# Optimization experiments

Hardware: AMD Instinct MI355X
Metric: run time of the kernel (lower is better)

The kernel has to match this reference:

```python
import jax, jax.numpy as jnp
import numpy as np

LAMBDA_DRO = 0.1
EPSILON = 0.5
EPS = 1e-8

N, M, D, K = 2048, 4096, 512, 1000


def _cosine_matrix(a, b):
    # a: [N, d], b: [M, d] -> [N, M] cosine similarity via normalize + GEMM
    an = a / jnp.maximum(jnp.linalg.norm(a, axis=1, keepdims=True), EPS)
    bn = b / jnp.maximum(jnp.linalg.norm(b, axis=1, keepdims=True), EPS)
    return an @ bn.T


def setup_inputs() -> dict:
    key = jax.random.key(0)
    k = jax.random.split(key, 7)
    return {
        "ptr_features": jax.random.normal(k[0], (N, D), dtype=jnp.float32),
        "ptr_logits": jax.random.normal(k[1], (N, K), dtype=jnp.float32),
        "ptr_labels": jax.random.randint(k[2], (N,), 0, K),
        "nu_features": jax.random.normal(k[3], (M, D), dtype=jnp.float32),
        "nu_logits": jax.random.normal(k[4], (M, K), dtype=jnp.float32),
        "nu_labels": jax.random.randint(k[5], (M,), 0, K),
        "classifier_weights": jax.random.normal(k[6], (K, D), dtype=jnp.float32),
    }


def reference(ptr_features, ptr_logits, ptr_labels, nu_features, nu_logits,
              nu_labels, classifier_weights):
    # per-sample CE loss on nu (hard labels)
    log_probs = jax.nn.log_softmax(nu_logits, axis=1)          # [M, K]
    nu_losses = -jnp.take_along_axis(log_probs, nu_labels[:, None], axis=1)[:, 0]  # [M]

    # transport costs
    C_X = 1.0 - _cosine_matrix(ptr_features, nu_features)       # [N, M]
    ptr_emb = classifier_weights[ptr_labels]                    # [N, d]
    nu_emb = classifier_weights[nu_labels]                      # [M, d]
    C_Y = 1.0 - _cosine_matrix(ptr_emb, nu_emb)                 # [N, M]
    C_total = C_X + C_Y

    # worst-case distribution Q^lambda
    exponent = (nu_losses[None, :] - LAMBDA_DRO * C_total) / (LAMBDA_DRO * EPSILON + EPS)
    exponent = exponent - jnp.max(exponent, axis=1, keepdims=True)
    exp_terms = jnp.exp(exponent)                               # [N, M]
    weights = exp_terms / (jnp.sum(exp_terms, axis=1, keepdims=True) + EPS)
    probs = jnp.mean(weights, axis=0)                           # [M]
    probs = probs / (jnp.sum(probs) + EPS)

    dro_loss = jnp.sum(probs * nu_losses)
    total_loss = dro_loss  # semantic_loss = 0 (no moco inputs)
    return (total_loss, dro_loss, probs, jnp.mean(C_total), jnp.mean(C_X), jnp.mean(C_Y))
```

## Files before the change

### kernel.cpp

```cpp
#include <hip/hip_runtime.h>
#include <math.h>

#define N_PTR 2048
#define M_NU  4096
#define DIM   512
#define KCLS  1000
#define KPAD  1024

static constexpr float LAMBDA_ = 0.1f;
static constexpr float EPS_ = 1e-8f;
static constexpr float INV_DENOM = 1.0f / (0.1f * 0.5f + 1e-8f);

typedef short short8 __attribute__((ext_vector_type(8)));
typedef unsigned short u16x8 __attribute__((ext_vector_type(8)));
typedef float f32x4 __attribute__((ext_vector_type(4)));

__device__ __forceinline__ unsigned short f2bf(float x) {
  unsigned u = __float_as_uint(x);
  u += 0x7fff + ((u >> 16) & 1);
  return (unsigned short)(u >> 16);
}
__device__ __forceinline__ float bf2f(unsigned short h) {
  return __uint_as_float(((unsigned)h) << 16);
}

__device__ __forceinline__ void gload16(const void* g, void* l) {
  __builtin_amdgcn_global_load_lds(
      (const __attribute__((address_space(1))) unsigned int*)g,
      (__attribute__((address_space(3))) unsigned int*)l, 16, 0, 0);
}

__device__ __forceinline__ float blk_reduce_sum(float v, float* red) {
  #pragma unroll
  for (int off = 32; off > 0; off >>= 1) v += __shfl_down(v, off);
  __syncthreads();
  if ((threadIdx.x & 63) == 0) red[threadIdx.x >> 6] = v;
  __syncthreads();
  return red[0] + red[1] + red[2] + red[3];
}

__device__ __forceinline__ float blk_reduce_max(float v, float* red) {
  #pragma unroll
  for (int off = 32; off > 0; off >>= 1) v = fmaxf(v, __shfl_down(v, off));
  __syncthreads();
  if ((threadIdx.x & 63) == 0) red[threadIdx.x >> 6] = v;
  __syncthreads();
  return fmaxf(fmaxf(red[0], red[1]), fmaxf(red[2], red[3]));
}

__global__ __launch_bounds__(256) void prep_kernel(
    const float* __restrict__ ptr_f, const float* __restrict__ nu_f,
    const float* __restrict__ cls_f, const float* __restrict__ logits,
    const int* __restrict__ labels, unsigned short* __restrict__ An,
    unsigned short* __restrict__ Bn, unsigned short* __restrict__ Cn,
    float* __restrict__ losses) {
  __shared__ float red[4];
  int b = blockIdx.x;
  if (b < 1792) {
    int gid = b * 256 + threadIdx.x;
    int row = gid >> 6, lane = gid & 63;
    const float* src; unsigned short* dst; int lrow; int in_rows;
    if (row < N_PTR)             { src = ptr_f; dst = An; lrow = row;                in_rows = N_PTR; }
    else if (row < N_PTR + M_NU) { src = nu_f;  dst = Bn; lrow = row - N_PTR;        in_rows = M_NU; }
    else                         { src = cls_f; dst = Cn; lrow = row - N_PTR - M_NU; in_rows = KCLS; }
    u16x8 ov;
    if (lrow < in_rows) {
      const float4* rp = (const float4*)(src + (size_t)lrow * DIM);
      float4 a = rp[lane * 2], bq = rp[lane * 2 + 1];
      float v[8] = {a.x, a.y, a.z, a.w, bq.x, bq.y, bq.z, bq.w};
      float s = 0.f;
      #pragma unroll
      for (int j = 0; j < 8; ++j) s = fmaf(v[j], v[j], s);
      #pragma unroll
      for (int off = 32; off > 0; off >>= 1) s += __shfl_xor(s, off);
      float inv = 1.0f / fmaxf(sqrtf(s), EPS_);
      #pragma unroll
      for (int j = 0; j < 8; ++j) ov[j] = f2bf(v[j] * inv);
    } else {
      #pragma unroll
      for (int j = 0; j < 8; ++j) ov[j] = 0;
    }
    *(u16x8*)(dst + (size_t)lrow * DIM + lane * 8) = ov;
  } else {
    int row = b - 1792;
    int tid = threadIdx.x;
    const float* x = logits + (size_t)row * KCLS;
    const float4* x4 = (const float4*)x;
    float4 v = make_float4(0.f, 0.f, 0.f, 0.f);
    float mx_loc = -INFINITY;
    if (tid < 250) {
      v = x4[tid];
      mx_loc = fmaxf(fmaxf(v.x, v.y), fmaxf(v.z, v.w));
    }
    float mx = blk_reduce_max(mx_loc, red);
    float se_loc = 0.f;
    if (tid < 250)
      se_loc = __expf(v.x - mx) + __expf(v.y - mx) + __expf(v.z - mx) + __expf(v.w - mx);
    float se = blk_reduce_sum(se_loc, red);
    if (tid == 0) losses[row] = mx + logf(se) - x[labels[row]];
  }
}

template <int BM, int MODE>
__global__ __launch_bounds__(256) void mfma_gemm(
    const unsigned short* __restrict__ A, const unsigned short* __restrict__ B,
    unsigned short* __restrict__ Gfb, unsigned short* __restrict__ Tb,
    const int* __restrict__ pl, const int* __restrict__ nl,
    const float* __restrict__ nu_loss, unsigned* __restrict__ gbits,
    float* __restrict__ pr, float* __restrict__ pr2,
    float* __restrict__ s_part, float* __restrict__ gy_part, int ldc) {
  constexpr int FR = BM / 32;
  constexpr int WSPAN = BM / 2;
  __shared__ unsigned short Alds[BM * 64];
  __shared__ unsigned short Blds[BM * 64];
  __shared__ float red[4];
  const int tid = threadIdx.x;
  const int w = tid >> 6, lane = tid & 63;
  const int brow = blockIdx.y * BM, bcol = blockIdx.x * BM;
  const int wr = w >> 1, wc = w & 1;

  if (MODE == 0 && blockIdx.x == 0 && blockIdx.y == 0) {
    float mloc = 0.f;
    for (int i = tid; i < M_NU; i += 256) mloc = fmaxf(mloc, nu_loss[i]);
    float mx = blk_reduce_max(mloc, red);
    if (tid == 0) *gbits = __float_as_uint(mx);
    __syncthreads();
  }

  const int sr = lane >> 3;
  const int sc = lane & 7;
  const int schunk = (sc ^ sr) * 8;

  f32x4 acc[FR][FR] = {};

  for (int k0 = 0; k0 < DIM; k0 += 64) {
    #pragma unroll
    for (int i = 0; i < FR; ++i) {
      int j = w * FR + i;
      int r = j * 8 + sr;
      gload16(A + (size_t)(brow + r) * DIM + k0 + schunk, (char*)Alds + j * 1024);
      gload16(B + (size_t)(bcol + r) * DIM + k0 + schunk, (char*)Blds + j * 1024);
    }
    __syncthreads();
    #pragma unroll
    for (int kk = 0; kk < 2; ++kk) {
      const int koff = kk * 64 + (lane >> 4) * 16;
      short8 af[FR], bfr[FR];
      #pragma unroll
      for (int mi = 0; mi < FR; ++mi) {
        int r = wr * WSPAN + mi * 16 + (lane & 15);
        af[mi] = *(const short8*)((const char*)Alds + r * 128 + (koff ^ ((r & 7) << 4)));
      }
      #pragma unroll
      for (int ni = 0; ni < FR; ++ni) {
        int r = wc * WSPAN + ni * 16 + (lane & 15);
        bfr[ni] = *(const short8*)((const char*)Blds + r * 128 + (koff ^ ((r & 7) << 4)));
      }
      #pragma unroll
      for (int mi = 0; mi < FR; ++mi)
        #pragma unroll
        for (int ni = 0; ni < FR; ++ni)
          acc[mi][ni] = __builtin_amdgcn_mfma_f32_16x16x32_bf16(af[mi], bfr[ni], acc[mi][ni], 0, 0, 0);
    }
    __syncthreads();
  }

  if (MODE == 0) {
    #pragma unroll
    for (int mi = 0; mi < FR; ++mi)
      #pragma unroll
      for (int ni = 0; ni < FR; ++ni)
        #pragma unroll
        for (int j = 0; j < 4; ++j) {
          int row = brow + wr * WSPAN + mi * 16 + (lane >> 4) * 4 + j;
          int col = bcol + wc * WSPAN + ni * 16 + (lane & 15);
          Gfb[(size_t)row * ldc + col] = f2bf(acc[mi][ni][j]);
        }
  } else {
    const float gmax = __uint_as_float(*gbits);
    const float fac = LAMBDA_ * INV_DENOM;
    int cols[FR]; float a_r[FR]; float loss_r[FR]; int nl_r[FR];
    #pragma unroll
    for (int ni = 0; ni < FR; ++ni) {
      cols[ni]  = bcol + wc * WSPAN + ni * 16 + (lane & 15);
      loss_r[ni] = nu_loss[cols[ni]];
      a_r[ni]   = (loss_r[ni] - gmax - 2.f * LAMBDA_) * INV_DENOM;
      nl_r[ni]  = nl[cols[ni]];
    }
    float s_acc = 0.f, gy_acc = 0.f;
    #pragma unroll
    for (int mi = 0; mi < FR; ++mi) {
      #pragma unroll
      for (int j = 0; j < 4; ++j) {
        int row = brow + wr * WSPAN + mi * 16 + (lane >> 4) * 4 + j;
        const unsigned short* Grow = Gfb + (size_t)pl[row] * KPAD;
        float rowacc = 0.f, rowacc2 = 0.f;
        #pragma unroll
        for (int ni = 0; ni < FR; ++ni) {
          float s  = acc[mi][ni][j];
          float gy = bf2f(Grow[nl_r[ni]]);
          float e  = fmaf(fac, s + gy, a_r[ni]);
          float t  = __expf(e);
          unsigned short tb = f2bf(t);
          Tb[(size_t)row * ldc + cols[ni]] = tb;
          float tt = bf2f(tb);
          rowacc  += tt;
          rowacc2 += tt * loss_r[ni];
          s_acc += s; gy_acc += gy;
        }
        #pragma unroll
        for (int off = 1; off < 16; off <<= 1) {
          rowacc  += __shfl_xor(rowacc, off);
          rowacc2 += __shfl_xor(rowacc2, off);
        }
        if ((lane & 15) == 0) {
          pr [(size_t)(blockIdx.x * 2 + wc) * N_PTR + row] = rowacc;
          pr2[(size_t)(blockIdx.x * 2 + wc) * N_PTR + row] = rowacc2;
        }
      }
    }
    float stot = blk_reduce_sum(s_acc, red);
    float gtot = blk_reduce_sum(gy_acc, red);
    if (tid == 0) {
      int bid = blockIdx.y * gridDim.x + blockIdx.x;
      s_part[bid] = stot; gy_part[bid] = gtot;
    }
  }
}

__global__ __launch_bounds__(256) void colpass_td_kernel(
    const unsigned short* __restrict__ Tb, const float* __restrict__ pr,
    const float* __restrict__ pr2, float* __restrict__ partial,
    float* __restrict__ T_part, float* __restrict__ D_part) {
  __shared__ float sh[64];
  int b = blockIdx.x, tid = threadIdx.x;
  if (b < 256) {
    int bx = b & 7, by = b >> 3;
    int m0 = bx * 512 + tid * 2;
    int n0 = by * 64;
    if (tid < 64) {
      float rs = 0.f;
      #pragma unroll 4
      for (int cb = 0; cb < 64; ++cb) rs += pr[(size_t)cb * N_PTR + n0 + tid];
      sh[tid] = 1.0f / (rs + EPS_);
    }
    __syncthreads();
    float a0 = 0.f, a1 = 0.f;
    #pragma unroll 4
    for (int i = 0; i < 64; ++i) {
      unsigned tv = *(const unsigned*)(Tb + (size_t)(n0 + i) * M_NU + m0);
      float wv = sh[i];
      a0 = fmaf(bf2f((unsigned short)(tv & 0xffffu)), wv, a0);
      a1 = fmaf(bf2f((unsigned short)(tv >> 16)), wv, a1);
    }
    *(float2*)(partial + (size_t)by * M_NU + m0) = make_float2(a0, a1);
  } else {
    int n = (b - 256) * 128 + (tid & 127);
    float tl = 0.f, dl = 0.f;
    if (tid < 128) {
      float rs = 0.f, wl = 0.f;
      #pragma unroll 4
      for (int cb = 0; cb < 64; ++cb) {
        rs += pr [(size_t)cb * N_PTR + n];
        wl += pr2[(size_t)cb * N_PTR + n];
      }
      float wi = 1.0f / (rs + EPS_);
      tl = rs * wi; dl = wl * wi;
    }
    __syncthreads();
    #pragma unroll
    for (int off = 32; off > 0; off >>= 1) { tl += __shfl_down(tl, off); dl += __shfl_down(dl, off); }
    if ((tid & 63) == 0) { sh[tid >> 6] = tl; sh[4 + (tid >> 6)] = dl; }
    __syncthreads();
    if (tid == 0) {
      T_part[b - 256] = sh[0] + sh[1] + sh[2] + sh[3];
      D_part[b - 256] = sh[4] + sh[5] + sh[6] + sh[7];
    }
  }
}

__global__ __launch_bounds__(256) void final_kernel(const float* __restrict__ partial,
    const float* __restrict__ T_part, const float* __restrict__ D_part,
    const float* __restrict__ s_part, const float* __restrict__ gy_part,
    float* __restrict__ out) {
  __shared__ float red[4];
  int b = blockIdx.x, tid = threadIdx.x;
  float T = 0.f;
  #pragma unroll
  for (int i = 0; i < 16; ++i) T += T_part[i];
  float scale = (1.0f / (float)N_PTR) / (T / (float)N_PTR + EPS_);
  if (b < 16) {
    int m = b * 256 + tid;
    float raw = 0.f;
    #pragma unroll
    for (int c = 0; c < 32; ++c) raw += partial[(size_t)c * M_NU + m];
    out[2 + m] = raw * scale;
  } else {
    float D = 0.f;
    #pragma unroll
    for (int i = 0; i < 16; ++i) D += D_part[i];
    float ls = 0.f, lg = 0.f;
    for (int i = tid; i < 512; i += 256) { ls += s_part[i]; lg += gy_part[i]; }
    float S  = blk_reduce_sum(ls, red);
    float Gy = blk_reduce_sum(lg, red);
    if (tid == 0) {
      float dro = D * scale;
      const float invNM = 1.0f / ((float)N_PTR * (float)M_NU);
      float mcx = 1.f - S * invNM;
      float mcy = 1.f - Gy * invNM;
      out[0] = dro;
      out[1] = dro;
      out[2 + M_NU] = mcx + mcy;
      out[3 + M_NU] = mcx;
      out[4 + M_NU] = mcy;
    }
  }
}

extern "C" void kernel_launch(void* const* d_in, const int* in_sizes, int n_in,
                              void* d_out, int out_size, void* d_ws, size_t ws_size,
                              hipStream_t stream) {
  const float* ptr_feat = (const float*)d_in[0];
  const int*   ptr_lab  = (const int*)d_in[2];
  const float* nu_feat  = (const float*)d_in[3];
  const float* nu_log   = (const float*)d_in[4];
  const int*   nu_lab   = (const int*)d_in[5];
  const float* cls_w    = (const float*)d_in[6];
  float* out = (float*)d_out;

  char* base = (char*)d_ws;
  unsigned short* Tb  = (unsigned short*)base;
  unsigned short* Gfb = (unsigned short*)(base + 16u * 1024 * 1024);
  unsigned short* An  = (unsigned short*)(base + 18u * 1024 * 1024);
  unsigned short* Bn  = (unsigned short*)(base + 20u * 1024 * 1024);
  unsigned short* Cn  = (unsigned short*)(base + 24u * 1024 * 1024);
  float* fb           = (float*)(base + 25u * 1024 * 1024);
  float* nloss   = fb;
  unsigned* gbits= (unsigned*)(nloss + 4096);
  float* pr      = nloss + 4096 + 64;
  float* pr2     = pr  + 64 * N_PTR;
  float* partial = pr2 + 64 * N_PTR;
  float* s_part  = partial + 32 * M_NU;
  float* gy_part = s_part + 512;
  float* T_part  = gy_part + 512;
  float* D_part  = T_part + 16;

  prep_kernel<<<dim3(1792 + M_NU), 256, 0, stream>>>(
      ptr_feat, nu_feat, cls_w, nu_log, nu_lab, An, Bn, Cn, nloss);
  mfma_gemm<64, 0><<<dim3(KPAD / 64, KPAD / 64), 256, 0, stream>>>(
      Cn, Cn, Gfb, nullptr, nullptr, nullptr, nloss, gbits,
      nullptr, nullptr, nullptr, nullptr, KPAD);
  mfma_gemm<128, 1><<<dim3(M_NU / 128, N_PTR / 128), 256, 0, stream>>>(
      An, Bn, Gfb, Tb, ptr_lab, nu_lab, nloss, gbits,
      pr, pr2, s_part, gy_part, M_NU);
  colpass_td_kernel<<<dim3(272), 256, 0, stream>>>(Tb, pr, pr2, partial, T_part, D_part);
  final_kernel<<<dim3(17), 256, 0, stream>>>(partial, T_part, D_part, s_part, gy_part, out);
}
```

Baseline: 62.79 us.

## Fold class-embedding cosine into main GEMM via concatenated K; compute means from column sums

Replaces the separate class-class Gram GEMM and per-element gathers of Gy with a gather of normalized class embeddings per sample (Ae, Be). The main GEMM then accumulates over both feature and embedding halves, giving S+Gy directly. The means of C_X and C_Y are computed from the dot product of column sums (sum_i a_i · sum_j b_j) in a small colsum kernel instead of in the GEMM epilogue. This removes the gathered bf16 lookups and the per-tile reductions from the epilogue, but doubles the GEMM K dimension and adds prep work for the 6144 gathered rows.

```diff
diff --git a/kernel.cpp b/kernel.cpp
--- a/kernel.cpp
+++ b/kernel.cpp
@@ -5,7 +5,6 @@
 #define M_NU  4096
 #define DIM   512
 #define KCLS  1000
-#define KPAD  1024
 
 static constexpr float LAMBDA_ = 0.1f;
 static constexpr float EPS_ = 1e-8f;
@@ -51,39 +50,45 @@
 __global__ __launch_bounds__(256) void prep_kernel(
     const float* __restrict__ ptr_f, const float* __restrict__ nu_f,
     const float* __restrict__ cls_f, const float* __restrict__ logits,
-    const int* __restrict__ labels, unsigned short* __restrict__ An,
-    unsigned short* __restrict__ Bn, unsigned short* __restrict__ Cn,
+    const int* __restrict__ pl, const int* __restrict__ nl,
+    const int* __restrict__ labels,
+    unsigned short* __restrict__ An, unsigned short* __restrict__ Bn,
+    unsigned short* __restrict__ Ae, unsigned short* __restrict__ Be,
     float* __restrict__ losses) {
   __shared__ float red[4];
   int b = blockIdx.x;
-  if (b < 1792) {
-    int gid = b * 256 + threadIdx.x;
+  int tid = threadIdx.x;
+  if (b < 3072) {
+    int gid = b * 256 + tid;
     int row = gid >> 6, lane = gid & 63;
-    const float* src; unsigned short* dst; int lrow; int in_rows;
-    if (row < N_PTR)             { src = ptr_f; dst = An; lrow = row;                in_rows = N_PTR; }
-    else if (row < N_PTR + M_NU) { src = nu_f;  dst = Bn; lrow = row - N_PTR;        in_rows = M_NU; }
-    else                         { src = cls_f; dst = Cn; lrow = row - N_PTR - M_NU; in_rows = KCLS; }
+    const float* src; unsigned short* dst;
+    if (row < N_PTR) {
+      src = ptr_f + (size_t)row * DIM;           dst = An + (size_t)row * DIM;
+    } else if (row < N_PTR + M_NU) {
+      int r = row - N_PTR;
+      src = nu_f + (size_t)r * DIM;              dst = Bn + (size_t)r * DIM;
+    } else if (row < N_PTR + M_NU + N_PTR) {
+      int r = row - N_PTR - M_NU;
+      src = cls_f + (size_t)pl[r] * DIM;         dst = Ae + (size_t)r * DIM;
+    } else {
+      int r = row - N_PTR - M_NU - N_PTR;
+      src = cls_f + (size_t)nl[r] * DIM;         dst = Be + (size_t)r * DIM;
+    }
+    const float4* rp = (const float4*)src;
+    float4 a = rp[lane * 2], bq = rp[lane * 2 + 1];
+    float v[8] = {a.x, a.y, a.z, a.w, bq.x, bq.y, bq.z, bq.w};
+    float s = 0.f;
+    #pragma unroll
+    for (int j = 0; j < 8; ++j) s = fmaf(v[j], v[j], s);
+    #pragma unroll
+    for (int off = 32; off > 0; off >>= 1) s += __shfl_xor(s, off);
+    float inv = 1.0f / fmaxf(sqrtf(s), EPS_);
     u16x8 ov;
-    if (lrow < in_rows) {
-      const float4* rp = (const float4*)(src + (size_t)lrow * DIM);
-      float4 a = rp[lane * 2], bq = rp[lane * 2 + 1];
-      float v[8] = {a.x, a.y, a.z, a.w, bq.x, bq.y, bq.z, bq.w};
-      float s = 0.f;
-      #pragma unroll
-      for (int j = 0; j < 8; ++j) s = fmaf(v[j], v[j], s);
-      #pragma unroll
-      for (int off = 32; off > 0; off >>= 1) s += __shfl_xor(s, off);
-      float inv = 1.0f / fmaxf(sqrtf(s), EPS_);
-      #pragma unroll
-      for (int j = 0; j < 8; ++j) ov[j] = f2bf(v[j] * inv);
-    } else {
-      #pragma unroll
-      for (int j = 0; j < 8; ++j) ov[j] = 0;
-    }
-    *(u16x8*)(dst + (size_t)lrow * DIM + lane * 8) = ov;
+    #pragma unroll
+    for (int j = 0; j < 8; ++j) ov[j] = f2bf(v[j] * inv);
+    *(u16x8*)(dst + lane * 8) = ov;
   } else {
-    int row = b - 1792;
-    int tid = threadIdx.x;
+    int row = b - 3072;
     const float* x = logits + (size_t)row * KCLS;
     const float4* x4 = (const float4*)x;
     float4 v = make_float4(0.f, 0.f, 0.f, 0.f);
@@ -101,129 +106,124 @@
   }
 }
 
-template <int BM, int MODE>
-__global__ __launch_bounds__(256) void mfma_gemm(
-    const unsigned short* __restrict__ A, const unsigned short* __restrict__ B,
-    unsigned short* __restrict__ Gfb, unsigned short* __restrict__ Tb,
-    const int* __restrict__ pl, const int* __restrict__ nl,
-    const float* __restrict__ nu_loss, unsigned* __restrict__ gbits,
-    float* __restrict__ pr, float* __restrict__ pr2,
-    float* __restrict__ s_part, float* __restrict__ gy_part, int ldc) {
-  constexpr int FR = BM / 32;
-  constexpr int WSPAN = BM / 2;
-  __shared__ unsigned short Alds[BM * 64];
-  __shared__ unsigned short Blds[BM * 64];
+__global__ __launch_bounds__(256) void colsum_kernel(
+    const unsigned short* __restrict__ An, const unsigned short* __restrict__ Bn,
+    const unsigned short* __restrict__ Ae, const unsigned short* __restrict__ Be,
+    const float* __restrict__ nloss, float* __restrict__ csum_part,
+    unsigned* __restrict__ gbits) {
   __shared__ float red[4];
+  int b = blockIdx.x, tid = threadIdx.x;
+  if (b == 96) {
+    float mloc = 0.f;
+    for (int i = tid; i < M_NU; i += 256) mloc = fmaxf(mloc, nloss[i]);
+    float mx = blk_reduce_max(mloc, red);
+    if (tid == 0) *gbits = __float_as_uint(mx);
+    return;
+  }
+  const unsigned short* basep; int n0;
+  if (b < 16)      { basep = An; n0 = b * 128; }
+  else if (b < 48) { basep = Bn; n0 = (b - 16) * 128; }
+  else if (b < 64) { basep = Ae; n0 = (b - 48) * 128; }
+  else             { basep = Be; n0 = (b - 64) * 128; }
+  float a0 = 0.f, a1 = 0.f;
+  for (int i = 0; i < 128; ++i) {
+    unsigned v = *(const unsigned*)(basep + (size_t)(n0 + i) * DIM + tid * 2);
+    a0 += bf2f((unsigned short)(v & 0xffffu));
+    a1 += bf2f((unsigned short)(v >> 16));
+  }
+  csum_part[(size_t)b * DIM + tid * 2]     = a0;
+  csum_part[(size_t)b * DIM + tid * 2 + 1] = a1;
+}
+
+__global__ __launch_bounds__(256) void sgemm_kernel(
+    const unsigned short* __restrict__ An, const unsigned short* __restrict__ Bn,
+    const unsigned short* __restrict__ Ae, const unsigned short* __restrict__ Be,
+    unsigned short* __restrict__ Tb, const int* __restrict__ nl,
+    const float* __restrict__ nu_loss, const unsigned* __restrict__ gbits,
+    float* __restrict__ pr, float* __restrict__ pr2) {
+  __shared__ unsigned short Alds[128 * 64];
+  __shared__ unsigned short Blds[128 * 64];
   const int tid = threadIdx.x;
   const int w = tid >> 6, lane = tid & 63;
-  const int brow = blockIdx.y * BM, bcol = blockIdx.x * BM;
+  const int brow = blockIdx.y * 128, bcol = blockIdx.x * 128;
   const int wr = w >> 1, wc = w & 1;
-
-  if (MODE == 0 && blockIdx.x == 0 && blockIdx.y == 0) {
-    float mloc = 0.f;
-    for (int i = tid; i < M_NU; i += 256) mloc = fmaxf(mloc, nu_loss[i]);
-    float mx = blk_reduce_max(mloc, red);
-    if (tid == 0) *gbits = __float_as_uint(mx);
-    __syncthreads();
-  }
 
   const int sr = lane >> 3;
   const int sc = lane & 7;
   const int schunk = (sc ^ sr) * 8;
 
-  f32x4 acc[FR][FR] = {};
-
-  for (int k0 = 0; k0 < DIM; k0 += 64) {
-    #pragma unroll
-    for (int i = 0; i < FR; ++i) {
-      int j = w * FR + i;
-      int r = j * 8 + sr;
-      gload16(A + (size_t)(brow + r) * DIM + k0 + schunk, (char*)Alds + j * 1024);
-      gload16(B + (size_t)(bcol + r) * DIM + k0 + schunk, (char*)Blds + j * 1024);
-    }
-    __syncthreads();
-    #pragma unroll
-    for (int kk = 0; kk < 2; ++kk) {
-      const int koff = kk * 64 + (lane >> 4) * 16;
-      short8 af[FR], bfr[FR];
+  f32x4 acc[4][4] = {};
+
+  #pragma unroll
+  for (int half = 0; half < 2; ++half) {
+    const unsigned short* Ab = half ? Ae : An;
+    const unsigned short* Bb = half ? Be : Bn;
+    for (int k0 = 0; k0 < DIM; k0 += 64) {
       #pragma unroll
-      for (int mi = 0; mi < FR; ++mi) {
-        int r = wr * WSPAN + mi * 16 + (lane & 15);
-        af[mi] = *(const short8*)((const char*)Alds + r * 128 + (koff ^ ((r & 7) << 4)));
-      }
+      for (int i = 0; i < 4; ++i) {
+        int j = w * 4 + i;
+        int r = j * 8 + sr;
+        gload16(Ab + (size_t)(brow + r) * DIM + k0 + schunk, (char*)Alds + j * 1024);
+        gload16(Bb + (size_t)(bcol + r) * DIM + k0 + schunk, (char*)Blds + j * 1024);
+      }
+      __syncthreads();
       #pragma unroll
-      for (int ni = 0; ni < FR; ++ni) {
-        int r = wc * WSPAN + ni * 16 + (lane & 15);
-        bfr[ni] = *(const short8*)((const char*)Blds + r * 128 + (koff ^ ((r & 7) << 4)));
-      }
-      #pragma unroll
-      for (int mi = 0; mi < FR; ++mi)
+      for (int kk = 0; kk < 2; ++kk) {
+        const int koff = kk * 64 + (lane >> 4) * 16;
+        short8 af[4], bfr[4];
         #pragma unroll
-        for (int ni = 0; ni < FR; ++ni)
-          acc[mi][ni] = __builtin_amdgcn_mfma_f32_16x16x32_bf16(af[mi], bfr[ni], acc[mi][ni], 0, 0, 0);
-    }
-    __syncthreads();
-  }
-
-  if (MODE == 0) {
-    #pragma unroll
-    for (int mi = 0; mi < FR; ++mi)
-      #pragma unroll
-      for (int ni = 0; ni < FR; ++ni)
-        #pragma unroll
-        for (int j = 0; j < 4; ++j) {
-          int row = brow + wr * WSPAN + mi * 16 + (lane >> 4) * 4 + j;
-          int col = bcol + wc * WSPAN + ni * 16 + (lane & 15);
-          Gfb[(size_t)row * ldc + col] = f2bf(acc[mi][ni][j]);
-        }
-  } else {
-    const float gmax = __uint_as_float(*gbits);
-    const float fac = LAMBDA_ * INV_DENOM;
-    int cols[FR]; float a_r[FR]; float loss_r[FR]; int nl_r[FR];
-    #pragma unroll
-    for (int ni = 0; ni < FR; ++ni) {
-      cols[ni]  = bcol + wc * WSPAN + ni * 16 + (lane & 15);
-      loss_r[ni] = nu_loss[cols[ni]];
-      a_r[ni]   = (loss_r[ni] - gmax - 2.f * LAMBDA_) * INV_DENOM;
-      nl_r[ni]  = nl[cols[ni]];
-    }
-    float s_acc = 0.f, gy_acc = 0.f;
-    #pragma unroll
-    for (int mi = 0; mi < FR; ++mi) {
-      #pragma unroll
-      for (int j = 0; j < 4; ++j) {
-        int row = brow + wr * WSPAN + mi * 16 + (lane >> 4) * 4 + j;
-        const unsigned short* Grow = Gfb + (size_t)pl[row] * KPAD;
-        float rowacc = 0.f, rowacc2 = 0.f;
-        #pragma unroll
-        for (int ni = 0; ni < FR; ++ni) {
-          float s  = acc[mi][ni][j];
-          float gy = bf2f(Grow[nl_r[ni]]);
-          float e  = fmaf(fac, s + gy, a_r[ni]);
-          float t  = __expf(e);
-          unsigned short tb = f2bf(t);
-          Tb[(size_t)row * ldc + cols[ni]] = tb;
-          float tt = bf2f(tb);
-          rowacc  += tt;
-          rowacc2 += tt * loss_r[ni];
-          s_acc += s; gy_acc += gy;
+        for (int mi = 0; mi < 4; ++mi) {
+          int r = wr * 64 + mi * 16 + (lane & 15);
+          af[mi] = *(const short8*)((const char*)Alds + r * 128 + (koff ^ ((r & 7) << 4)));
         }
         #pragma unroll
-        for (int off = 1; off < 16; off <<= 1) {
-          rowacc  += __shfl_xor(rowacc, off);
-          rowacc2 += __shfl_xor(rowacc2, off);
+        for (int ni = 0; ni < 4; ++ni) {
+          int r = wc * 64 + ni * 16 + (lane & 15);
+          bfr[ni] = *(const short8*)((const char*)Blds + r * 128 + (koff ^ ((r & 7) << 4)));
         }
-        if ((lane & 15) == 0) {
-          pr [(size_t)(blockIdx.x * 2 + wc) * N_PTR + row] = rowacc;
-          pr2[(size_t)(blockIdx.x * 2 + wc) * N_PTR + row] = rowacc2;
-        }
-      }
-    }
-    float stot = blk_reduce_sum(s_acc, red);
-    float gtot = blk_reduce_sum(gy_acc, red);
-    if (tid == 0) {
-      int bid = blockIdx.y * gridDim.x + blockIdx.x;
-      s_part[bid] = stot; gy_part[bid] = gtot;
+        #pragma unroll
+        for (int mi = 0; mi < 4; ++mi)
+          #pragma unroll
+          for (int ni = 0; ni < 4; ++ni)
+            acc[mi][ni] = __builtin_amdgcn_mfma_f32_16x16x32_bf16(af[mi], bfr[ni], acc[mi][ni], 0, 0, 0);
+      }
+      __syncthreads();
+    }
+  }
+
+  const float gmax = __uint_as_float(*gbits);
+  const float fac = LAMBDA_ * INV_DENOM;
+  int cols[4]; float a_r[4]; float loss_r[4];
+  #pragma unroll
+  for (int ni = 0; ni < 4; ++ni) {
+    cols[ni]   = bcol + wc * 64 + ni * 16 + (lane & 15);
+    loss_r[ni] = nu_loss[cols[ni]];
+    a_r[ni]    = (loss_r[ni] - gmax - 2.f * LAMBDA_) * INV_DENOM;
+  }
+  #pragma unroll
+  for (int mi = 0; mi < 4; ++mi) {
+    #pragma unroll
+    for (int j = 0; j < 4; ++j) {
+      int row = brow + wr * 64 + mi * 16 + (lane >> 4) * 4 + j;
+      float rowacc = 0.f, rowacc2 = 0.f;
+      #pragma unroll
+      for (int ni = 0; ni < 4; ++ni) {
+        float t = __expf(fmaf(fac, acc[mi][ni][j], a_r[ni]));
+        unsigned short tb = f2bf(t);
+        Tb[(size_t)row * M_NU + cols[ni]] = tb;
+        float tt = bf2f(tb);
+        rowacc  += tt;
+        rowacc2 += tt * loss_r[ni];
+      }
+      #pragma unroll
+      for (int off = 1; off < 16; off <<= 1) {
+        rowacc  += __shfl_xor(rowacc, off);
+        rowacc2 += __shfl_xor(rowacc2, off);
+      }
+      if ((lane & 15) == 0) {
+        pr [(size_t)(blockIdx.x * 2 + wc) * N_PTR + row] = rowacc;
+        pr2[(size_t)(blockIdx.x * 2 + wc) * N_PTR + row] = rowacc2;
+      }
     }
   }
 }
@@ -281,8 +281,7 @@
 
 __global__ __launch_bounds__(256) void final_kernel(const float* __restrict__ partial,
     const float* __restrict__ T_part, const float* __restrict__ D_part,
-    const float* __restrict__ s_part, const float* __restrict__ gy_part,
-    float* __restrict__ out) {
+    const float* __restrict__ csum_part, float* __restrict__ out) {
   __shared__ float red[4];
   int b = blockIdx.x, tid = threadIdx.x;
   float T = 0.f;
@@ -299,15 +298,27 @@
     float D = 0.f;
     #pragma unroll
     for (int i = 0; i < 16; ++i) D += D_part[i];
-    float ls = 0.f, lg = 0.f;
-    for (int i = tid; i < 512; i += 256) { ls += s_part[i]; lg += gy_part[i]; }
-    float S  = blk_reduce_sum(ls, red);
-    float Gy = blk_reduce_sum(lg, red);
+    float lx = 0.f, ly = 0.f;
+    for (int c = tid; c < DIM; c += 256) {
+      float sA = 0.f, sB = 0.f, sPe = 0.f, sQe = 0.f;
+      #pragma unroll 4
+      for (int p = 0; p < 16; ++p)  sA  += csum_part[(size_t)p * DIM + c];
+      #pragma unroll 4
+      for (int p = 16; p < 48; ++p) sB  += csum_part[(size_t)p * DIM + c];
+      #pragma unroll 4
+      for (int p = 48; p < 64; ++p) sPe += csum_part[(size_t)p * DIM + c];
+      #pragma unroll 4
+      for (int p = 64; p < 96; ++p) sQe += csum_part[(size_t)p * DIM + c];
+      lx = fmaf(sA, sB, lx);
+      ly = fmaf(sPe, sQe, ly);
+    }
+    float dX = blk_reduce_sum(lx, red);
+    float dY = blk_reduce_sum(ly, red);
     if (tid == 0) {
       float dro = D * scale;
       const float invNM = 1.0f / ((float)N_PTR * (float)M_NU);
-      float mcx = 1.f - S * invNM;
-      float mcy = 1.f - Gy * invNM;
+      float mcx = 1.f - dX * invNM;
+      float mcy = 1.f - dY * invNM;
       out[0] = dro;
       out[1] = dro;
       out[2 + M_NU] = mcx + mcy;
@@ -329,30 +340,27 @@
   float* out = (float*)d_out;
 
   char* base = (char*)d_ws;
-  unsigned short* Tb  = (unsigned short*)base;
-  unsigned short* Gfb = (unsigned short*)(base + 16u * 1024 * 1024);
-  unsigned short* An  = (unsigned short*)(base + 18u * 1024 * 1024);
-  unsigned short* Bn  = (unsigned short*)(base + 20u * 1024 * 1024);
-  unsigned short* Cn  = (unsigned short*)(base + 24u * 1024 * 1024);
-  float* fb           = (float*)(base + 25u * 1024 * 1024);
-  float* nloss   = fb;
-  unsigned* gbits= (unsigned*)(nloss + 4096);
-  float* pr      = nloss + 4096 + 64;
-  float* pr2     = pr  + 64 * N_PTR;
-  float* partial = pr2 + 64 * N_PTR;
-  float* s_part  = partial + 32 * M_NU;
-  float* gy_part = s_part + 512;
-  float* T_part  = gy_part + 512;
-  float* D_part  = T_part + 16;
-
-  prep_kernel<<<dim3(1792 + M_NU), 256, 0, stream>>>(
-      ptr_feat, nu_feat, cls_w, nu_log, nu_lab, An, Bn, Cn, nloss);
-  mfma_gemm<64, 0><<<dim3(KPAD / 64, KPAD / 64), 256, 0, stream>>>(
-      Cn, Cn, Gfb, nullptr, nullptr, nullptr, nloss, gbits,
-      nullptr, nullptr, nullptr, nullptr, KPAD);
-  mfma_gemm<128, 1><<<dim3(M_NU / 128, N_PTR / 128), 256, 0, stream>>>(
-      An, Bn, Gfb, Tb, ptr_lab, nu_lab, nloss, gbits,
-      pr, pr2, s_part, gy_part, M_NU);
+  unsigned short* Tb = (unsigned short*)base;
+  unsigned short* An = (unsigned short*)(base + 16u * 1024 * 1024);
+  unsigned short* Bn = (unsigned short*)(base + 18u * 1024 * 1024);
+  unsigned short* Ae = (unsigned short*)(base + 22u * 1024 * 1024);
+  unsigned short* Be = (unsigned short*)(base + 24u * 1024 * 1024);
+  float* fb          = (float*)(base + 28u * 1024 * 1024);
+  float* nloss     = fb;
+  unsigned* gbits  = (unsigned*)(nloss + 4096);
+  float* pr        = nloss + 4096 + 64;
+  float* pr2       = pr  + 64 * N_PTR;
+  float* partial   = pr2 + 64 * N_PTR;
+  float* T_part    = partial + 32 * M_NU;
+  float* D_part    = T_part + 16;
+  float* csum_part = D_part + 48;
+
+  prep_kernel<<<dim3(3072 + M_NU), 256, 0, stream>>>(
+      ptr_feat, nu_feat, cls_w, nu_log, ptr_lab, nu_lab, nu_lab,
+      An, Bn, Ae, Be, nloss);
+  colsum_kernel<<<dim3(97), 256, 0, stream>>>(An, Bn, Ae, Be, nloss, csum_part, gbits);
+  sgemm_kernel<<<dim3(M_NU / 128, N_PTR / 128), 256, 0, stream>>>(
+      An, Bn, Ae, Be, Tb, nu_lab, nloss, gbits, pr, pr2);
   colpass_td_kernel<<<dim3(272), 256, 0, stream>>>(Tb, pr, pr2, partial, T_part, D_part);
-  final_kernel<<<dim3(17), 256, 0, stream>>>(partial, T_part, D_part, s_part, gy_part, out);
-}
+  final_kernel<<<dim3(17), 256, 0, stream>>>(partial, T_part, D_part, csum_part, out);
+}
```

After: 76.73 us. +22.2%, slower.
